# Kernel tuning notes

Measured on AMD Instinct MI355X. Metric: run time of the kernel, lower is better.

## Reference

```python
import jax, jax.numpy as jnp
import numpy as np

TEMPERATURE = 0.2
EPS = 1e-12


def setup_inputs() -> dict:
    key = jax.random.key(0)
    k1, k2 = jax.random.split(key)
    x = jax.random.normal(k1, (16384, 2048), dtype=jnp.float32)
    protos = jax.random.normal(k2, (4096, 2048), dtype=jnp.float32)
    # buffer is initialized as row-normalized in the torch module
    protos = protos / jnp.maximum(jnp.linalg.norm(protos, axis=1, keepdims=True), EPS)
    return {"x": x, "prototypes": protos, "k": 16}


def reference(x, prototypes, k):
    # L2-normalize inputs (torch F.normalize uses eps clamp on the norm)
    xn = x / jnp.maximum(jnp.linalg.norm(x, axis=-1, keepdims=True), EPS)
    # cosine similarities: (B, P)
    sims = jnp.einsum("bd,pd->bp", xn, prototypes)
    topk_vals, topk_idx = jax.lax.top_k(sims, k)          # (B, k)
    topk_softmax = jax.nn.softmax(topk_vals / TEMPERATURE, axis=-1)
    rows = jnp.arange(sims.shape[0])[:, None]             # (B, 1)
    sparse_act = jnp.zeros_like(sims).at[rows, topk_idx].set(topk_softmax)
    return sparse_act
```

## Files before the change

### kernel.cpp

```cpp
#include <hip/hip_runtime.h>
#include <hip/hip_bf16.h>
#include <stdint.h>

typedef __attribute__((ext_vector_type(8))) short bf16x8;
typedef __attribute__((ext_vector_type(4))) float f32x4;
typedef unsigned short u16;

#define M_ROWS 16384
#define N_COLS 4096
#define K_DIM  2048
#define TOPK   16
#define KSEL   16
#define CAP    48
#define INV_T  5.0f
#define DELTA  0.05f

#define BM 128
#define BN 128
#define BK 64
#define NKT (K_DIM / BK)

__device__ __forceinline__ void async_cp16(const void* g, void* l) {
  __builtin_amdgcn_global_load_lds((const __attribute__((address_space(1))) uint32_t*)g,
                                   (__attribute__((address_space(3))) uint32_t*)l,
                                   16, 0, 0);
}

__device__ __forceinline__ u16 f2bf(float f) {
  __hip_bfloat16 h = __float2bfloat16(f);
  return *reinterpret_cast<u16*>(&h);
}
__device__ __forceinline__ uint2 pack4(float4 v) {
  uint2 r;
  r.x = (uint32_t)f2bf(v.x) | ((uint32_t)f2bf(v.y) << 16);
  r.y = (uint32_t)f2bf(v.z) | ((uint32_t)f2bf(v.w) << 16);
  return r;
}

__global__ __launch_bounds__(256) void prep_x_kernel(
    const float* __restrict__ x, u16* __restrict__ xh, float* __restrict__ invn) {
  const int row = blockIdx.x;
  const int t = threadIdx.x;
  const float4* xr = reinterpret_cast<const float4*>(x + (size_t)row * K_DIM);
  float4 v0 = xr[t];
  float4 v1 = xr[256 + t];
  float s = v0.x*v0.x + v0.y*v0.y + v0.z*v0.z + v0.w*v0.w
          + v1.x*v1.x + v1.y*v1.y + v1.z*v1.z + v1.w*v1.w;
  #pragma unroll
  for (int off = 1; off < 64; off <<= 1) s += __shfl_xor(s, off);
  __shared__ float ws4[4];
  if ((t & 63) == 0) ws4[t >> 6] = s;
  __syncthreads();
  if (t == 0) {
    float tot = ws4[0] + ws4[1] + ws4[2] + ws4[3];
    invn[row] = 1.0f / fmaxf(sqrtf(tot), 1e-12f);
  }
  uint2* xo = reinterpret_cast<uint2*>(xh + (size_t)row * K_DIM);
  xo[t] = pack4(v0);
  xo[256 + t] = pack4(v1);
}

__global__ __launch_bounds__(256) void prep_p_kernel(
    const float* __restrict__ p, u16* __restrict__ ph) {
  const int row = blockIdx.x;
  const int t = threadIdx.x;
  const float4* pr = reinterpret_cast<const float4*>(p + (size_t)row * K_DIM);
  uint2* po = reinterpret_cast<uint2*>(ph + (size_t)row * K_DIM);
  po[t] = pack4(pr[t]);
  po[256 + t] = pack4(pr[256 + t]);
}

__global__ __launch_bounds__(256) void gemm_bf16_kernel(
    const u16* __restrict__ A, const u16* __restrict__ B, float* __restrict__ C) {
  __shared__ __align__(16) u16 sA[2][BM * BK];
  __shared__ __align__(16) u16 sB[2][BN * BK];
  const int t = threadIdx.x;
  const int lane = t & 63;
  const int wid = t >> 6;
  const int wm = wid >> 1, wn = wid & 1;
  const int tm0 = blockIdx.y * BM;
  const int tn0 = blockIdx.x * BN;
  const int lr = lane & 15;
  const int hi = lane >> 4;

  f32x4 acc[4][4];
  #pragma unroll
  for (int i = 0; i < 4; ++i)
    #pragma unroll
    for (int j = 0; j < 4; ++j)
      acc[i][j] = (f32x4){0.f, 0.f, 0.f, 0.f};

  int srow[4], soff[4];
  #pragma unroll
  for (int i = 0; i < 4; ++i) {
    int c = i * 256 + t;
    int r = c >> 3;
    int ib = (c & 7) << 4;
    srow[i] = r;
    soff[i] = ib ^ ((r & 7) << 4);
  }
  const char* Abase = (const char*)(A + (size_t)tm0 * K_DIM);
  const char* Bbase = (const char*)(B + (size_t)tn0 * K_DIM);

#define STAGE(slot, kt_) do {                                                 \
    const int kb_ = (kt_) * (BK * 2);                                         \
    _Pragma("unroll")                                                         \
    for (int i = 0; i < 4; ++i) {                                             \
      async_cp16(Abase + (size_t)srow[i] * (K_DIM * 2) + kb_ + soff[i],       \
                 (char*)sA[slot] + (i * 256 + t) * 16);                       \
      async_cp16(Bbase + (size_t)srow[i] * (K_DIM * 2) + kb_ + soff[i],       \
                 (char*)sB[slot] + (i * 256 + t) * 16);                       \
    }                                                                         \
  } while (0)

  STAGE(0, 0);
  STAGE(1, 1);

  for (int kt = 0; kt < NKT; ++kt) {
    if (kt + 1 < NKT) asm volatile("s_waitcnt vmcnt(8)" ::: "memory");
    else              asm volatile("s_waitcnt vmcnt(0)" ::: "memory");
    __builtin_amdgcn_sched_barrier(0);
    __builtin_amdgcn_s_barrier();
    asm volatile("" ::: "memory");

    const char* cA = (const char*)sA[kt & 1];
    const char* cB = (const char*)sB[kt & 1];
    bf16x8 af[4][2], bq[4][2];
    #pragma unroll
    for (int f = 0; f < 4; ++f) {
      #pragma unroll
      for (int kk = 0; kk < 2; ++kk) {
        int rowA = wm * 64 + f * 16 + lr;
        int inbA = (kk * 64 + (hi << 4)) ^ ((rowA & 7) << 4);
        af[f][kk] = *reinterpret_cast<const bf16x8*>(cA + rowA * 128 + inbA);
        int rowB = wn * 64 + f * 16 + lr;
        int inbB = (kk * 64 + (hi << 4)) ^ ((rowB & 7) << 4);
        bq[f][kk] = *reinterpret_cast<const bf16x8*>(cB + rowB * 128 + inbB);
      }
    }
    asm volatile("s_waitcnt lgkmcnt(0)" ::: "memory");
    __builtin_amdgcn_sched_barrier(0);
    if (kt + 2 < NKT) {
      __builtin_amdgcn_s_barrier();
      asm volatile("" ::: "memory");
      __builtin_amdgcn_sched_barrier(0);
      STAGE(kt & 1, kt + 2);
    }
    __builtin_amdgcn_s_setprio(1);
    #pragma unroll
    for (int kk = 0; kk < 2; ++kk)
      #pragma unroll
      for (int i = 0; i < 4; ++i)
        #pragma unroll
        for (int j = 0; j < 4; ++j)
          acc[i][j] = __builtin_amdgcn_mfma_f32_16x16x32_bf16(
              af[i][kk], bq[j][kk], acc[i][j], 0, 0, 0);
    __builtin_amdgcn_s_setprio(0);
  }
#undef STAGE

  #pragma unroll
  for (int i = 0; i < 4; ++i) {
    #pragma unroll
    for (int j = 0; j < 4; ++j) {
      int colg = tn0 + wn * 64 + j * 16 + lr;
      int rowb = tm0 + wm * 64 + i * 16 + (hi << 2);
      #pragma unroll
      for (int r = 0; r < 4; ++r) {
        __builtin_nontemporal_store(acc[i][j][r], &C[(size_t)(rowb + r) * N_COLS + colg]);
      }
    }
  }
}

__global__ __launch_bounds__(256) void topk_kernel(
    const float* __restrict__ x, const float* __restrict__ protos,
    const float* __restrict__ invn, float* __restrict__ out) {
  const int row = blockIdx.x;
  const int t = threadIdx.x;
  const int lane = t & 63;
  const int wid = t >> 6;

  __shared__ __align__(16) f32x4 lx[512];
  __shared__ int hist[4][257];
  __shared__ int selInfo[2];
  __shared__ int   wtotC[4], wtotW[4];
  __shared__ int   cposC[16];
  __shared__ float cargC[16];
  __shared__ int   wpos[CAP];
  __shared__ float cexact[CAP];
  __shared__ int   spos[TOPK];
  __shared__ float sval[TOPK];

  float* orow = out + (size_t)row * N_COLS;
  const f32x4* orow4 = reinterpret_cast<const f32x4*>(orow);

  f32x4 sv[4];
  uint32_t key[16];
  #pragma unroll
  for (int i = 0; i < 4; ++i) {
    sv[i] = __builtin_nontemporal_load(orow4 + i * 256 + t);
    #pragma unroll
    for (int c = 0; c < 4; ++c) {
      uint32_t u = __float_as_uint(sv[i][c]);
      key[i * 4 + c] = (u & 0x80000000u) ? ~u : (u | 0x80000000u);
    }
  }

  const f32x4* xr = reinterpret_cast<const f32x4*>(x + (size_t)row * K_DIM);
  lx[t] = __builtin_nontemporal_load(xr + t);
  lx[256 + t] = __builtin_nontemporal_load(xr + 256 + t);

  uint32_t prefix = 0;
  int K_rem = KSEL;
  #pragma unroll
  for (int pass = 0; pass < 4; ++pass) {
    const int shift = 24 - pass * 8;
    hist[0][t] = 0; hist[1][t] = 0; hist[2][t] = 0; hist[3][t] = 0;
    __syncthreads();
    const uint32_t prefMask = (pass == 0) ? 0u : (0xFFFFFFFFu << (shift + 8));
    #pragma unroll
    for (int j = 0; j < 16; ++j) {
      if ((key[j] & prefMask) == prefix)
        atomicAdd(&hist[wid][(key[j] >> shift) & 255], 1);
    }
    __syncthreads();
    if (wid == 0) {
      const int b0 = lane << 2;
      int h0 = hist[0][b0]     + hist[1][b0]     + hist[2][b0]     + hist[3][b0];
      int h1 = hist[0][b0 + 1] + hist[1][b0 + 1] + hist[2][b0 + 1] + hist[3][b0 + 1];
      int h2 = hist[0][b0 + 2] + hist[1][b0 + 2] + hist[2][b0 + 2] + hist[3][b0 + 2];
      int h3 = hist[0][b0 + 3] + hist[1][b0 + 3] + hist[2][b0 + 3] + hist[3][b0 + 3];
      int loc = h0 + h1 + h2 + h3;
      int s = loc;
      #pragma unroll
      for (int off = 1; off < 64; off <<= 1) {
        int o = __shfl_down(s, off);
        if (lane + off < 64) s += o;
      }
      const int tail = s - loc;
      int s3 = tail + h3;
      int s2 = s3 + h2;
      int s1 = s2 + h1;
      int s0 = s1 + h0;
      int ge[4] = {s0, s1, s2, s3};
      int hh[4] = {h0, h1, h2, h3};
      #pragma unroll
      for (int k = 0; k < 4; ++k) {
        int gt = ge[k] - hh[k];
        if (gt < K_rem && ge[k] >= K_rem) {
          selInfo[0] = b0 + k;
          selInfo[1] = K_rem - gt;
        }
      }
    }
    __syncthreads();
    prefix |= ((uint32_t)selInfo[0]) << shift;
    K_rem = selInfo[1];
  }
  const uint32_t T = prefix;
  const float a16 = __uint_as_float((T & 0x80000000u) ? (T ^ 0x80000000u) : ~T);
  const float vhi = a16 + DELTA;
  const float vlo = a16 - DELTA;
  const float inv = invn[row];

  int lcC = 0, lcW = 0;
  #pragma unroll
  for (int j = 0; j < 16; ++j) {
    float v = sv[j >> 2][j & 3];
    if (v > vhi) ++lcC;
    else if (v >= vlo) ++lcW;
  }
  int pC = lcC, pW = lcW;
  #pragma unroll
  for (int off = 1; off < 64; off <<= 1) {
    int oC = __shfl_up(pC, off);
    int oW = __shfl_up(pW, off);
    if (lane >= off) { pC += oC; pW += oW; }
  }
  if (lane == 63) { wtotC[wid] = pC; wtotW[wid] = pW; }
  __syncthreads();
  int baseC = pC - lcC, baseW = pW - lcW;
  for (int w2 = 0; w2 < wid; ++w2) { baseC += wtotC[w2]; baseW += wtotW[w2]; }
  const int m  = wtotC[0] + wtotC[1] + wtotC[2] + wtotC[3];
  const int wc = min(wtotW[0] + wtotW[1] + wtotW[2] + wtotW[3], CAP);
  #pragma unroll
  for (int j = 0; j < 16; ++j) {
    float v = sv[j >> 2][j & 3];
    int pos = ((j >> 2) << 10) + (t << 2) + (j & 3);
    if (v > vhi) { cposC[baseC] = pos; cargC[baseC] = v; ++baseC; }
    else if (v >= vlo) { if (baseW < CAP) { wpos[baseW] = pos; ++baseW; } }
  }
  __syncthreads();

  for (int ci = wid; ci < wc; ci += 4) {
    int pidx = wpos[ci];
    const f32x4* pr = reinterpret_cast<const f32x4*>(protos + (size_t)pidx * K_DIM);
    float s = 0.f;
    #pragma unroll
    for (int i = 0; i < 8; ++i) {
      f32x4 pv = pr[i * 64 + lane];
      f32x4 xv = lx[i * 64 + lane];
      s = fmaf(pv.x, xv.x, s);
      s = fmaf(pv.y, xv.y, s);
      s = fmaf(pv.z, xv.z, s);
      s = fmaf(pv.w, xv.w, s);
    }
    #pragma unroll
    for (int off = 1; off < 64; off <<= 1) s += __shfl_xor(s, off);
    if (lane == 0) cexact[ci] = s * inv;
  }
  __syncthreads();

  if (wid == 0) {
    const int w_need = TOPK - m;
    float v = (lane < wc) ? cexact[lane] : -3.0e38f;
    int pos = (lane < wc) ? wpos[lane] : 0x7fffffff;
    int rank = 0;
    for (int j = 0; j < wc; ++j) {
      float vj = __shfl(v, j);
      int   pj = __shfl(pos, j);
      if (lane < wc && j != lane)
        if (vj > v || (vj == v && pj < pos)) rank++;
    }
    bool sel = (lane < wc) && (rank < w_need);
    unsigned long long bal = __ballot(sel);
    int slot = __popcll(bal & ((1ull << lane) - 1ull));
    if (sel) { spos[m + slot] = pos; sval[m + slot] = v; }
    if (lane < m) { spos[lane] = cposC[lane]; sval[lane] = cargC[lane] * inv; }
    float av = (lane < TOPK) ? sval[lane] : -3.0e38f;
    float vm = av;
    #pragma unroll
    for (int off = 1; off < 16; off <<= 1) vm = fmaxf(vm, __shfl_xor(vm, off));
    float e = (lane < TOPK) ? expf((av - vm) * INV_T) : 0.f;
    float se = e;
    #pragma unroll
    for (int off = 1; off < 16; off <<= 1) se += __shfl_xor(se, off);
    if (lane < TOPK) sval[lane] = e / se;
  }
  __syncthreads();

  f32x4* orow4w = reinterpret_cast<f32x4*>(orow);
  #pragma unroll
  for (int i = 0; i < 4; ++i) {
    f32x4 o = (f32x4){0.f, 0.f, 0.f, 0.f};
    #pragma unroll
    for (int s = 0; s < TOPK; ++s) {
      int p = spos[s];
      if ((p >> 10) == i && ((p >> 2) & 255) == t) o[p & 3] = sval[s];
    }
    __builtin_nontemporal_store(o, orow4w + i * 256 + t);
  }
}

extern "C" void kernel_launch(void* const* d_in, const int* in_sizes, int n_in,
                              void* d_out, int out_size, void* d_ws, size_t ws_size,
                              hipStream_t stream) {
  const float* x = (const float*)d_in[0];
  const float* protos = (const float*)d_in[1];
  float* out = (float*)d_out;

  char* ws = (char*)d_ws;
  u16* xh = (u16*)ws;
  u16* ph = (u16*)(ws + (size_t)M_ROWS * K_DIM * 2);
  float* invn = (float*)(ws + (size_t)(M_ROWS + N_COLS) * K_DIM * 2);

  prep_x_kernel<<<M_ROWS, 256, 0, stream>>>(x, xh, invn);
  prep_p_kernel<<<N_COLS, 256, 0, stream>>>(protos, ph);

  dim3 gg(N_COLS / BN, M_ROWS / BM);
  gemm_bf16_kernel<<<gg, 256, 0, stream>>>(xh, ph, out);

  topk_kernel<<<M_ROWS, 256, 0, stream>>>(x, protos, invn, out);
}
```

Measured before the change: 566.4 us.

## Split GEMM LDS fragment loads into halves and move output scatter to writer kernel

In the GEMM main loop, the LDS fragment loads are split into two k-halves. A partial lgkmcnt wait lets MFMAs on the first half start while the second-half loads are still in flight. Separately, the top-k kernel now writes its 16 indices and softmax weights to workspace, which overwrites the bf16 prototype buffer after the GEMM no longer needs it. A new writer kernel then fills each output row. This adds a kernel launch and a small extra global round trip in exchange for a simpler top-k kernel tail.

```diff
diff --git a/kernel.cpp b/kernel.cpp
--- a/kernel.cpp
+++ b/kernel.cpp
@@ -125,19 +125,36 @@
 
     const char* cA = (const char*)sA[kt & 1];
     const char* cB = (const char*)sB[kt & 1];
-    bf16x8 af[4][2], bq[4][2];
+    bf16x8 af0[4], bq0[4], af1[4], bq1[4];
     #pragma unroll
     for (int f = 0; f < 4; ++f) {
+      int rowA = wm * 64 + f * 16 + lr;
+      int rowB = wn * 64 + f * 16 + lr;
+      af0[f] = *reinterpret_cast<const bf16x8*>(
+          cA + rowA * 128 + ((hi << 4) ^ ((rowA & 7) << 4)));
+      bq0[f] = *reinterpret_cast<const bf16x8*>(
+          cB + rowB * 128 + ((hi << 4) ^ ((rowB & 7) << 4)));
+    }
+    __builtin_amdgcn_sched_barrier(0);
+    #pragma unroll
+    for (int f = 0; f < 4; ++f) {
+      int rowA = wm * 64 + f * 16 + lr;
+      int rowB = wn * 64 + f * 16 + lr;
+      af1[f] = *reinterpret_cast<const bf16x8*>(
+          cA + rowA * 128 + ((64 + (hi << 4)) ^ ((rowA & 7) << 4)));
+      bq1[f] = *reinterpret_cast<const bf16x8*>(
+          cB + rowB * 128 + ((64 + (hi << 4)) ^ ((rowB & 7) << 4)));
+    }
+    asm volatile("s_waitcnt lgkmcnt(8)" ::: "memory");
+    __builtin_amdgcn_sched_barrier(0);
+    __builtin_amdgcn_s_setprio(1);
+    #pragma unroll
+    for (int i = 0; i < 4; ++i)
       #pragma unroll
-      for (int kk = 0; kk < 2; ++kk) {
-        int rowA = wm * 64 + f * 16 + lr;
-        int inbA = (kk * 64 + (hi << 4)) ^ ((rowA & 7) << 4);
-        af[f][kk] = *reinterpret_cast<const bf16x8*>(cA + rowA * 128 + inbA);
-        int rowB = wn * 64 + f * 16 + lr;
-        int inbB = (kk * 64 + (hi << 4)) ^ ((rowB & 7) << 4);
-        bq[f][kk] = *reinterpret_cast<const bf16x8*>(cB + rowB * 128 + inbB);
-      }
-    }
+      for (int j = 0; j < 4; ++j)
+        acc[i][j] = __builtin_amdgcn_mfma_f32_16x16x32_bf16(
+            af0[i], bq0[j], acc[i][j], 0, 0, 0);
+    __builtin_amdgcn_s_setprio(0);
     asm volatile("s_waitcnt lgkmcnt(0)" ::: "memory");
     __builtin_amdgcn_sched_barrier(0);
     if (kt + 2 < NKT) {
@@ -148,13 +165,11 @@
     }
     __builtin_amdgcn_s_setprio(1);
     #pragma unroll
-    for (int kk = 0; kk < 2; ++kk)
+    for (int i = 0; i < 4; ++i)
       #pragma unroll
-      for (int i = 0; i < 4; ++i)
-        #pragma unroll
-        for (int j = 0; j < 4; ++j)
-          acc[i][j] = __builtin_amdgcn_mfma_f32_16x16x32_bf16(
-              af[i][kk], bq[j][kk], acc[i][j], 0, 0, 0);
+      for (int j = 0; j < 4; ++j)
+        acc[i][j] = __builtin_amdgcn_mfma_f32_16x16x32_bf16(
+            af1[i], bq1[j], acc[i][j], 0, 0, 0);
     __builtin_amdgcn_s_setprio(0);
   }
 #undef STAGE
@@ -175,7 +190,8 @@
 
 __global__ __launch_bounds__(256) void topk_kernel(
     const float* __restrict__ x, const float* __restrict__ protos,
-    const float* __restrict__ invn, float* __restrict__ out) {
+    const float* __restrict__ invn, const float* __restrict__ sims,
+    int* __restrict__ sposg, float* __restrict__ svalg) {
   const int row = blockIdx.x;
   const int t = threadIdx.x;
   const int lane = t & 63;
@@ -192,8 +208,7 @@
   __shared__ int   spos[TOPK];
   __shared__ float sval[TOPK];
 
-  float* orow = out + (size_t)row * N_COLS;
-  const f32x4* orow4 = reinterpret_cast<const f32x4*>(orow);
+  const f32x4* orow4 = reinterpret_cast<const f32x4*>(sims + (size_t)row * N_COLS);
 
   f32x4 sv[4];
   uint32_t key[16];
@@ -336,18 +351,33 @@
     float se = e;
     #pragma unroll
     for (int off = 1; off < 16; off <<= 1) se += __shfl_xor(se, off);
-    if (lane < TOPK) sval[lane] = e / se;
+    if (lane < TOPK) {
+      sposg[(size_t)row * TOPK + lane] = spos[lane];
+      svalg[(size_t)row * TOPK + lane] = e / se;
+    }
+  }
+}
+
+__global__ __launch_bounds__(256) void writer_kernel(
+    const int* __restrict__ sposg, const float* __restrict__ svalg,
+    float* __restrict__ out) {
+  const int row = blockIdx.x;
+  const int t = threadIdx.x;
+  __shared__ int sp[TOPK];
+  __shared__ float svv[TOPK];
+  if (t < TOPK) {
+    sp[t] = sposg[(size_t)row * TOPK + t];
+    svv[t] = svalg[(size_t)row * TOPK + t];
   }
   __syncthreads();
-
-  f32x4* orow4w = reinterpret_cast<f32x4*>(orow);
+  f32x4* orow4w = reinterpret_cast<f32x4*>(out + (size_t)row * N_COLS);
   #pragma unroll
   for (int i = 0; i < 4; ++i) {
     f32x4 o = (f32x4){0.f, 0.f, 0.f, 0.f};
     #pragma unroll
     for (int s = 0; s < TOPK; ++s) {
-      int p = spos[s];
-      if ((p >> 10) == i && ((p >> 2) & 255) == t) o[p & 3] = sval[s];
+      int p = sp[s];
+      if ((p >> 10) == i && ((p >> 2) & 255) == t) o[p & 3] = svv[s];
     }
     __builtin_nontemporal_store(o, orow4w + i * 256 + t);
   }
@@ -364,6 +394,8 @@
   u16* xh = (u16*)ws;
   u16* ph = (u16*)(ws + (size_t)M_ROWS * K_DIM * 2);
   float* invn = (float*)(ws + (size_t)(M_ROWS + N_COLS) * K_DIM * 2);
+  int*   sposg = (int*)(ws + (size_t)M_ROWS * K_DIM * 2);
+  float* svalg = (float*)(ws + (size_t)M_ROWS * K_DIM * 2 + (size_t)M_ROWS * TOPK * 4);
 
   prep_x_kernel<<<M_ROWS, 256, 0, stream>>>(x, xh, invn);
   prep_p_kernel<<<N_COLS, 256, 0, stream>>>(protos, ph);
@@ -371,5 +403,6 @@
   dim3 gg(N_COLS / BN, M_ROWS / BM);
   gemm_bf16_kernel<<<gg, 256, 0, stream>>>(xh, ph, out);
 
-  topk_kernel<<<M_ROWS, 256, 0, stream>>>(x, protos, invn, out);
-}
+  topk_kernel<<<M_ROWS, 256, 0, stream>>>(x, protos, invn, out, sposg, svalg);
+  writer_kernel<<<M_ROWS, 256, 0, stream>>>(sposg, svalg, out);
+}
```

New measurement: 566.6 us. Within noise of the previous version (+0.0%).
